# Kernel tuning notes

Hardware: AMD Instinct MI355X
Metric: run time of the kernel (lower is better)

## Reference

```python
import jax, jax.numpy as jnp
import numpy as np

NEG_SLOPE = 0.2  # leaky_relu negative slope (alpha)

def _glorot(key, shape):
    fan_in, fan_out = shape[0], shape[-1]
    lim = jnp.sqrt(6.0 / (fan_in + fan_out))
    return jax.random.uniform(key, shape, jnp.float32, -lim, lim)

def setup_inputs() -> dict:
    key = jax.random.key(0)
    ks = jax.random.split(key, 10)
    N, E, F_IN, HID, HEADS, NCLASS = 50000, 800000, 512, 32, 8, 32
    x = jax.random.normal(ks[0], (N, F_IN), jnp.float32)
    edge_index = jax.random.randint(ks[1], (2, E), 0, N, jnp.int64)
    # layer 1: heads=8, out per head = 32, concat -> 256
    W1 = _glorot(ks[2], (F_IN, HEADS * HID))
    att_src1 = _glorot(ks[3], (HEADS, HID))
    att_dst1 = _glorot(ks[4], (HEADS, HID))
    b1 = jnp.zeros((HEADS * HID,), jnp.float32)
    # layer 2: heads=1, out = nclass
    W2 = _glorot(ks[5], (HEADS * HID, NCLASS))
    att_src2 = _glorot(ks[6], (1, NCLASS))
    att_dst2 = _glorot(ks[7], (1, NCLASS))
    b2 = jnp.zeros((NCLASS,), jnp.float32)
    return {"x": x, "edge_index": edge_index, "W1": W1, "att_src1": att_src1,
            "att_dst1": att_dst1, "b1": b1, "W2": W2, "att_src2": att_src2,
            "att_dst2": att_dst2, "b2": b2}

def gat_conv(x, src, dst, W, a_src, a_dst, bias, num_nodes):
    """PyG GATConv (eval mode, self loops already appended to src/dst)."""
    H, C = a_src.shape
    h = (x @ W).reshape(num_nodes, H, C)                 # [N,H,C]
    score_src = jnp.einsum('nhc,hc->nh', h, a_src)       # [N,H]
    score_dst = jnp.einsum('nhc,hc->nh', h, a_dst)       # [N,H]
    e = jax.nn.leaky_relu(score_src[src] + score_dst[dst], NEG_SLOPE)  # [E,H]
    m = jax.ops.segment_max(e, dst, num_segments=num_nodes)           # [N,H]
    w = jnp.exp(e - m[dst])
    denom = jax.ops.segment_sum(w, dst, num_segments=num_nodes)       # [N,H]
    alpha = w / (denom[dst] + 1e-16)                                  # [E,H]
    out = jax.ops.segment_sum(alpha[:, :, None] * h[src], dst,
                              num_segments=num_nodes)                 # [N,H,C]
    return out.reshape(num_nodes, H * C) + bias

def reference(x, edge_index, W1, att_src1, att_dst1, b1, W2, att_src2, att_dst2, b2):
    N = x.shape[0]
    loops = jnp.arange(N, dtype=edge_index.dtype)
    src = jnp.concatenate([edge_index[0], loops])  # PyG add_self_loops=True
    dst = jnp.concatenate([edge_index[1], loops])
    h = jax.nn.elu(gat_conv(x, src, dst, W1, att_src1, att_dst1, b1, N))
    out = gat_conv(h, src, dst, W2, att_src2, att_dst2, b2, N)
    return out + 1e-06
```

## Files before the change

### kernel.cpp

```cpp
#include <hip/hip_runtime.h>
#include <math.h>

#define N_NODES 50000
#define N_EDGES 800000
#define E2 (N_EDGES + N_NODES)
#define F_IN 512
#define HEADS 8
#define HID 32
#define HC 256
#define NCLASS 32
#define NEG_SLOPE 0.2f
#define ELLW 64

typedef unsigned int uint;
typedef unsigned short ushort;
typedef __attribute__((ext_vector_type(8))) short bf16x8;
typedef __attribute__((ext_vector_type(4))) float f32x4;

#define GLOBAL_LOAD_LDS16(g, l) \
    __builtin_amdgcn_global_load_lds((const __attribute__((address_space(1))) void*)(g), \
                                     (__attribute__((address_space(3))) void*)(l), 16, 0, 0)

__device__ inline uint bf16_rne_bits(float f) {
    uint u = __float_as_uint(f);
    return (u + 0x7fffu + ((u >> 16) & 1u)) >> 16;
}
__device__ inline float bf2f(ushort u) { return __uint_as_float(((uint)u) << 16); }

#define W1_BLOCKS 512
#define W2_BLOCKS 32
#define FILL_BLOCKS ((E2 / 4 + 255) / 256)

__global__ void __launch_bounds__(256) prep_kernel(const float* __restrict__ W1,
        ushort* __restrict__ w1hi, ushort* __restrict__ w1lo,
        const float* __restrict__ W2, ushort* __restrict__ w2hi, ushort* __restrict__ w2lo,
        const int* __restrict__ ei, int* __restrict__ cursor, int* __restrict__ ell) {
    int b = blockIdx.x;
    if (b < W1_BLOCKS) {
        int t = b * 256 + threadIdx.x;
        int n = t >> 9, k = t & 511;
        float f = W1[k * 256 + n];
        uint h = bf16_rne_bits(f);
        float r = f - __uint_as_float(h << 16);
        w1hi[t] = (ushort)h;
        w1lo[t] = (ushort)bf16_rne_bits(r);
    } else if (b < W1_BLOCKS + W2_BLOCKS) {
        int t = (b - W1_BLOCKS) * 256 + threadIdx.x;
        int n = t >> 8, k = t & 255;
        float f = W2[k * 32 + n];
        uint h = bf16_rne_bits(f);
        float r = f - __uint_as_float(h << 16);
        w2hi[t] = (ushort)h;
        w2lo[t] = (ushort)bf16_rne_bits(r);
    } else {
        int e0 = ((b - W1_BLOCKS - W2_BLOCKS) * 256 + threadIdx.x) * 4;
        if (e0 < E2) {
            int src[4], dst[4];
            if (e0 < N_EDGES) {
                int4 s4 = *(const int4*)(ei + e0);
                int4 d4 = *(const int4*)(ei + N_EDGES + e0);
                src[0] = s4.x; src[1] = s4.y; src[2] = s4.z; src[3] = s4.w;
                dst[0] = d4.x; dst[1] = d4.y; dst[2] = d4.z; dst[3] = d4.w;
            } else {
                #pragma unroll
                for (int j = 0; j < 4; ++j) { src[j] = e0 + j - N_EDGES; dst[j] = src[j]; }
            }
            #pragma unroll
            for (int j = 0; j < 4; ++j) {
                int d = dst[j];
                int p = atomicAdd(&cursor[d], 1);
                ell[d * ELLW + p] = src[j];
            }
        }
    }
}

__global__ void __launch_bounds__(256, 4) gemm1_mfma_kernel(const uint* __restrict__ xp,
        const ushort* __restrict__ bhi, const ushort* __restrict__ blo,
        const float* __restrict__ as1, const float* __restrict__ ad1,
        ushort* __restrict__ C, float* __restrict__ ssrc, float* __restrict__ sdst, int M) {
    __shared__ uint   As[64 * 32];
    __shared__ ushort Bh[128 * 32];
    __shared__ ushort Bl[128 * 32];
    const int tid = threadIdx.x, lane = tid & 63, wave = tid >> 6;

    const int NW = ((N_NODES + 63) / 64) * 2;
    const int orig = blockIdx.y * gridDim.x + blockIdx.x;
    const int xcd = orig & 7, idx = orig >> 3;
    const int q = NW >> 3, r = NW & 7;
    const int nid = (xcd < r ? xcd * (q + 1) : r * (q + 1) + (xcd - r) * q) + idx;
    const int bm = (nid >> 1) * 64, bn = (nid & 1) * 128;

    const uint* agp[2]; const uint* alp[2];
    #pragma unroll
    for (int s = 0; s < 2; ++s) {
        int t = wave * 2 + s;
        int p = t * 64 + lane;
        int row = p >> 3, cs = p & 7;
        int c = cs ^ (row & 7);
        int grow = bm + row; if (grow > M - 1) grow = M - 1;
        agp[s] = xp + ((size_t)grow * 512 + c * 4);
        alp[s] = &As[t * 256];
    }
    const ushort* bhgp[2]; const ushort* blgp[2]; const ushort* bhlp[2]; const ushort* bllp[2];
    #pragma unroll
    for (int s = 0; s < 2; ++s) {
        int t = wave * 2 + s;
        int p = t * 64 + lane;
        int row = p >> 2, qs = p & 3;
        int qq = qs ^ ((row >> 1) & 3);
        size_t go = (size_t)(bn + row) * 512 + qq * 8;
        bhgp[s] = bhi + go; blgp[s] = blo + go;
        bhlp[s] = &Bh[t * 512]; bllp[s] = &Bl[t * 512];
    }

    f32x4 acc[2][4] = {};
    const int wm = (wave >> 1) * 32, wn = (wave & 1) * 64;
    const int fm = lane & 15, quad = lane >> 4;

    for (int kk = 0; kk < 16; ++kk) {
        #pragma unroll
        for (int s = 0; s < 2; ++s) GLOBAL_LOAD_LDS16(agp[s], alp[s]);
        #pragma unroll
        for (int s = 0; s < 2; ++s) {
            GLOBAL_LOAD_LDS16(bhgp[s], bhlp[s]);
            GLOBAL_LOAD_LDS16(blgp[s], bllp[s]);
        }
        #pragma unroll
        for (int s = 0; s < 2; ++s) { agp[s] += 32; bhgp[s] += 32; blgp[s] += 32; }
        __syncthreads();

        bf16x8 ah[2], al[2], bh[4], bl[4];
        #pragma unroll
        for (int i = 0; i < 2; ++i) {
            int row = wm + i * 16 + fm;
            int sw = row & 7;
            uint4 c0 = *(const uint4*)&As[row * 32 + (((2 * quad)     ^ sw) * 4)];
            uint4 c1 = *(const uint4*)&As[row * 32 + (((2 * quad + 1) ^ sw) * 4)];
            union { uint u[4]; bf16x8 v; } H, L;
            H.u[0] = __builtin_amdgcn_perm(c0.y, c0.x, 0x07060302u);
            H.u[1] = __builtin_amdgcn_perm(c0.w, c0.z, 0x07060302u);
            H.u[2] = __builtin_amdgcn_perm(c1.y, c1.x, 0x07060302u);
            H.u[3] = __builtin_amdgcn_perm(c1.w, c1.z, 0x07060302u);
            uint r0 = __float_as_uint(__uint_as_float(c0.x) - __uint_as_float(c0.x & 0xffff0000u));
            uint r1 = __float_as_uint(__uint_as_float(c0.y) - __uint_as_float(c0.y & 0xffff0000u));
            uint r2 = __float_as_uint(__uint_as_float(c0.z) - __uint_as_float(c0.z & 0xffff0000u));
            uint r3 = __float_as_uint(__uint_as_float(c0.w) - __uint_as_float(c0.w & 0xffff0000u));
            uint r4 = __float_as_uint(__uint_as_float(c1.x) - __uint_as_float(c1.x & 0xffff0000u));
            uint r5 = __float_as_uint(__uint_as_float(c1.y) - __uint_as_float(c1.y & 0xffff0000u));
            uint r6 = __float_as_uint(__uint_as_float(c1.z) - __uint_as_float(c1.z & 0xffff0000u));
            uint r7 = __float_as_uint(__uint_as_float(c1.w) - __uint_as_float(c1.w & 0xffff0000u));
            L.u[0] = __builtin_amdgcn_perm(r1, r0, 0x07060302u);
            L.u[1] = __builtin_amdgcn_perm(r3, r2, 0x07060302u);
            L.u[2] = __builtin_amdgcn_perm(r5, r4, 0x07060302u);
            L.u[3] = __builtin_amdgcn_perm(r7, r6, 0x07060302u);
            ah[i] = H.v; al[i] = L.v;
        }
        #pragma unroll
        for (int j = 0; j < 4; ++j) {
            int row = wn + j * 16 + fm;
            int qs = quad ^ ((row >> 1) & 3);
            bh[j] = *(const bf16x8*)&Bh[row * 32 + qs * 8];
            bl[j] = *(const bf16x8*)&Bl[row * 32 + qs * 8];
        }
        #pragma unroll
        for (int i = 0; i < 2; ++i)
            #pragma unroll
            for (int j = 0; j < 4; ++j) {
                acc[i][j] = __builtin_amdgcn_mfma_f32_16x16x32_bf16(ah[i], bh[j], acc[i][j], 0, 0, 0);
                acc[i][j] = __builtin_amdgcn_mfma_f32_16x16x32_bf16(ah[i], bl[j], acc[i][j], 0, 0, 0);
                acc[i][j] = __builtin_amdgcn_mfma_f32_16x16x32_bf16(al[i], bh[j], acc[i][j], 0, 0, 0);
            }
        __syncthreads();
    }

    #pragma unroll
    for (int i = 0; i < 2; ++i) {
        int rb = bm + wm + i * 16 + quad * 4;
        #pragma unroll
        for (int j = 0; j < 4; ++j) {
            int col = bn + wn + j * 16 + fm;
            #pragma unroll
            for (int r2_ = 0; r2_ < 4; ++r2_) {
                int row = rb + r2_;
                if (row < M) C[(size_t)row * 256 + col] = (ushort)bf16_rne_bits(acc[i][j][r2_]);
            }
        }
    }

    const int head0 = (bn + wn) >> 5;
    const float asA0 = as1[head0 * 32 + fm],      asA1 = as1[head0 * 32 + 16 + fm];
    const float asB0 = as1[head0 * 32 + 32 + fm], asB1 = as1[head0 * 32 + 48 + fm];
    const float adA0 = ad1[head0 * 32 + fm],      adA1 = ad1[head0 * 32 + 16 + fm];
    const float adB0 = ad1[head0 * 32 + 32 + fm], adB1 = ad1[head0 * 32 + 48 + fm];
    #pragma unroll
    for (int i = 0; i < 2; ++i) {
        #pragma unroll
        for (int r2_ = 0; r2_ < 4; ++r2_) {
            int row = bm + wm + i * 16 + quad * 4 + r2_;
            float s1A = acc[i][0][r2_] * asA0 + acc[i][1][r2_] * asA1;
            float s1B = acc[i][2][r2_] * asB0 + acc[i][3][r2_] * asB1;
            float s2A = acc[i][0][r2_] * adA0 + acc[i][1][r2_] * adA1;
            float s2B = acc[i][2][r2_] * adB0 + acc[i][3][r2_] * adB1;
            #pragma unroll
            for (int off = 1; off < 16; off <<= 1) {
                s1A += __shfl_xor(s1A, off);
                s1B += __shfl_xor(s1B, off);
                s2A += __shfl_xor(s2A, off);
                s2B += __shfl_xor(s2B, off);
            }
            if (fm == 0 && row < M) {
                ssrc[(size_t)row * 8 + head0]     = s1A;
                ssrc[(size_t)row * 8 + head0 + 1] = s1B;
                sdst[(size_t)row * 8 + head0]     = s2A;
                sdst[(size_t)row * 8 + head0 + 1] = s2B;
            }
        }
    }
}

__global__ void __launch_bounds__(256) gemm2_mfma_kernel(const ushort* __restrict__ A,
        const ushort* __restrict__ bh_g, const ushort* __restrict__ bl_g,
        const float* __restrict__ as2, const float* __restrict__ ad2,
        ushort* __restrict__ C, float* __restrict__ ssrc, float* __restrict__ sdst, int M) {
    const int tid = threadIdx.x, lane = tid & 63, wave = tid >> 6;
    const int bm = blockIdx.x * 128;
    const int fm = lane & 15, quad = lane >> 4;
    const int wrow = wave * 32;

    int gr[2];
    #pragma unroll
    for (int i = 0; i < 2; ++i) {
        gr[i] = bm + wrow + i * 16 + fm;
        if (gr[i] > M - 1) gr[i] = M - 1;
    }

    f32x4 acc[2][2] = {};
    for (int kk = 0; kk < 8; ++kk) {
        bf16x8 a[2], bh[2], bl[2];
        #pragma unroll
        for (int i = 0; i < 2; ++i)
            a[i] = *(const bf16x8*)(A + (size_t)gr[i] * 256 + kk * 32 + quad * 8);
        #pragma unroll
        for (int j = 0; j < 2; ++j) {
            size_t off = (size_t)(j * 16 + fm) * 256 + kk * 32 + quad * 8;
            bh[j] = *(const bf16x8*)(bh_g + off);
            bl[j] = *(const bf16x8*)(bl_g + off);
        }
        #pragma unroll
        for (int i = 0; i < 2; ++i)
            #pragma unroll
            for (int j = 0; j < 2; ++j) {
                acc[i][j] = __builtin_amdgcn_mfma_f32_16x16x32_bf16(a[i], bh[j], acc[i][j], 0, 0, 0);
                acc[i][j] = __builtin_amdgcn_mfma_f32_16x16x32_bf16(a[i], bl[j], acc[i][j], 0, 0, 0);
            }
    }

    float a0 = as2[fm], a1 = as2[16 + fm];
    float d0 = ad2[fm], d1 = ad2[16 + fm];
    #pragma unroll
    for (int i = 0; i < 2; ++i) {
        #pragma unroll
        for (int r2_ = 0; r2_ < 4; ++r2_) {
            int rg = bm + wrow + i * 16 + quad * 4 + r2_;
            float v0 = acc[i][0][r2_], v1 = acc[i][1][r2_];
            float s1 = v0 * a0 + v1 * a1;
            float s2 = v0 * d0 + v1 * d1;
            #pragma unroll
            for (int off = 1; off < 16; off <<= 1) {
                s1 += __shfl_xor(s1, off);
                s2 += __shfl_xor(s2, off);
            }
            if (rg < M) {
                C[(size_t)rg * 32 + fm]      = (ushort)bf16_rne_bits(v0);
                C[(size_t)rg * 32 + 16 + fm] = (ushort)bf16_rne_bits(v1);
                if (fm == 0) { ssrc[rg] = s1; sdst[rg] = s2; }
            }
        }
    }
}

__global__ void __launch_bounds__(256) agg1_wave_kernel(const ushort* __restrict__ h,
        const float* __restrict__ ssrc, const float* __restrict__ sdst,
        const int* __restrict__ cnt, const int* __restrict__ ell,
        const float* __restrict__ bias, ushort* __restrict__ out) {
    const int wid = (blockIdx.x * blockDim.x + threadIdx.x) >> 6;
    if (wid >= N_NODES) return;
    const int lane = threadIdx.x & 63;
    const int hg = lane >> 3;
    const int hl = lane & 7;
    const int n = wid;
    const int beg = n * ELLW;
    const int end = beg + cnt[n];
    const float sdst_n = sdst[(size_t)n * HEADS + hg];

    float4 acc = make_float4(0.f, 0.f, 0.f, 0.f);
    float sw = 0.f;
    const ushort* hc = h + lane * 4;
    const int base = hg << 3;
    for (int e = beg; e < end; e += 16) {
        int ee0 = e + hl, ee1 = e + 8 + hl;
        int ei0 = ee0 < end ? ee0 : end - 1;
        int ei1 = ee1 < end ? ee1 : end - 1;
        int s0 = ell[ei0];
        int s1 = ell[ei1];
        float c0 = ssrc[(size_t)s0 * HEADS + hg] + sdst_n;
        float c1 = ssrc[(size_t)s1 * HEADS + hg] + sdst_n;
        c0 = c0 > 0.f ? c0 : NEG_SLOPE * c0;
        c1 = c1 > 0.f ? c1 : NEG_SLOPE * c1;
        float w0 = (ee0 < end) ? __expf(c0) : 0.f;
        float w1 = (ee1 < end) ? __expf(c1) : 0.f;
        float wj[16]; int sj[16];
        #pragma unroll
        for (int j = 0; j < 8; ++j) {
            wj[j]     = __shfl(w0, base + j);
            sj[j]     = __shfl(s0, base + j);
            wj[8 + j] = __shfl(w1, base + j);
            sj[8 + j] = __shfl(s1, base + j);
        }
        ushort4 v[16];
        #pragma unroll
        for (int j = 0; j < 16; ++j) v[j] = *(const ushort4*)(hc + (size_t)sj[j] * HC);
        #pragma unroll
        for (int j = 0; j < 16; ++j) {
            acc.x += wj[j] * bf2f(v[j].x);
            acc.y += wj[j] * bf2f(v[j].y);
            acc.z += wj[j] * bf2f(v[j].z);
            acc.w += wj[j] * bf2f(v[j].w);
            sw += wj[j];
        }
    }
    float inv = 1.f / (sw + 1e-16f);
    float4 bv = *(const float4*)(bias + lane * 4);
    float4 o;
    o.x = acc.x * inv + bv.x; o.y = acc.y * inv + bv.y;
    o.z = acc.z * inv + bv.z; o.w = acc.w * inv + bv.w;
    o.x = o.x > 0.f ? o.x : expm1f(o.x);
    o.y = o.y > 0.f ? o.y : expm1f(o.y);
    o.z = o.z > 0.f ? o.z : expm1f(o.z);
    o.w = o.w > 0.f ? o.w : expm1f(o.w);
    ushort4 ob;
    ob.x = (ushort)bf16_rne_bits(o.x);
    ob.y = (ushort)bf16_rne_bits(o.y);
    ob.z = (ushort)bf16_rne_bits(o.z);
    ob.w = (ushort)bf16_rne_bits(o.w);
    *(ushort4*)(out + (size_t)n * HC + lane * 4) = ob;
}

__global__ void __launch_bounds__(256) agg2_kernel(const ushort* __restrict__ h2,
        const float* __restrict__ ssrc, const float* __restrict__ sdst,
        const int* __restrict__ cnt, const int* __restrict__ ell,
        const float* __restrict__ bias, float* __restrict__ out) {
    const int n = blockIdx.x * 4 + (threadIdx.x >> 6);
    if (n >= N_NODES) return;
    const int beg = n * ELLW;
    const int end = beg + cnt[n];
    const int t = threadIdx.x & 63;
    const float sdst_n = sdst[n];

    const int slot = t >> 4, cp = t & 15;
    float a0 = 0.f, a1 = 0.f, sw = 0.f;
    for (int e = beg + slot; e < end; e += 4) {
        int src = ell[e];
        float sc = ssrc[src] + sdst_n;
        sc = sc > 0.f ? sc : NEG_SLOPE * sc;
        float w = __expf(sc);
        uint v = *(const uint*)(h2 + (size_t)src * NCLASS + cp * 2);
        a0 += w * __uint_as_float(v << 16);
        a1 += w * __uint_as_float(v & 0xffff0000u);
        sw += w;
    }
    a0 += __shfl_down(a0, 32); a1 += __shfl_down(a1, 32); sw += __shfl_down(sw, 32);
    a0 += __shfl_down(a0, 16); a1 += __shfl_down(a1, 16); sw += __shfl_down(sw, 16);
    if (t < 16) {
        float inv = 1.f / (sw + 1e-16f);
        float2 o;
        o.x = a0 * inv + bias[cp * 2]     + 1e-6f;
        o.y = a1 * inv + bias[cp * 2 + 1] + 1e-6f;
        *(float2*)(out + (size_t)n * NCLASS + cp * 2) = o;
    }
}

extern "C" void kernel_launch(void* const* d_in, const int* in_sizes, int n_in,
                              void* d_out, int out_size, void* d_ws, size_t ws_size,
                              hipStream_t stream) {
    const float* x        = (const float*)d_in[0];
    const int*   ei       = (const int*)  d_in[1];
    const float* W1       = (const float*)d_in[2];
    const float* att_src1 = (const float*)d_in[3];
    const float* att_dst1 = (const float*)d_in[4];
    const float* b1       = (const float*)d_in[5];
    const float* W2       = (const float*)d_in[6];
    const float* att_src2 = (const float*)d_in[7];
    const float* att_dst2 = (const float*)d_in[8];
    const float* b2       = (const float*)d_in[9];
    float* out = (float*)d_out;

    ushort* w1t_hi = (ushort*)d_ws;
    ushort* w1t_lo = w1t_hi + 256 * 512;
    ushort* w2t_hi = w1t_lo + 256 * 512;
    ushort* w2t_lo = w2t_hi + 32 * 256;
    ushort* h1b    = w2t_lo + 32 * 256;
    ushort* h2b    = h1b + (size_t)N_NODES * HC;
    ushort* out1b  = h2b + (size_t)N_NODES * NCLASS;
    float* ssrc1 = (float*)(out1b + (size_t)N_NODES * HC);
    float* sdst1 = ssrc1 + (size_t)N_NODES * HEADS;
    float* ssrc2 = sdst1 + (size_t)N_NODES * HEADS;
    float* sdst2 = ssrc2 + N_NODES;
    int* cursor  = (int*)(sdst2 + N_NODES);
    int* ell     = cursor + N_NODES;

    hipMemsetAsync(cursor, 0, N_NODES * sizeof(int), stream);
    prep_kernel<<<W1_BLOCKS + W2_BLOCKS + FILL_BLOCKS, 256, 0, stream>>>(
            W1, w1t_hi, w1t_lo, W2, w2t_hi, w2t_lo, ei, cursor, ell);

    {
        dim3 grid((N_NODES + 63) / 64, 2);
        gemm1_mfma_kernel<<<grid, 256, 0, stream>>>((const uint*)x, w1t_hi, w1t_lo,
                att_src1, att_dst1, h1b, ssrc1, sdst1, N_NODES);
    }
    agg1_wave_kernel<<<(N_NODES + 3) / 4, 256, 0, stream>>>(h1b, ssrc1, sdst1, cursor, ell, b1, out1b);

    gemm2_mfma_kernel<<<(N_NODES + 127) / 128, 256, 0, stream>>>(out1b, w2t_hi, w2t_lo,
            att_src2, att_dst2, h2b, ssrc2, sdst2, N_NODES);
    agg2_kernel<<<(N_NODES + 3) / 4, 256, 0, stream>>>(h2b, ssrc2, sdst2, cursor, ell, b2, out);
}
```

Measured before the change: 374.9 us.

## Enlarge GEMM1 tile, shrink GEMM2 tile, split agg1 tail loop

GEMM1 moves from 64x256-column tiles to 128-row tiles, so each wave computes a 64x64 sub-block and each loaded B tile is reused across twice as many rows, and the occupancy hint of 4 is dropped. GEMM2 goes the other way: each wave handles 16 rows instead of 32 and twice as many blocks are launched, giving more parallelism for the small 32-column output. The layer-1 aggregation loop is split into a mask-free main body over full 16-edge chunks plus a guarded tail that loads only the edges still needed, avoiding clamped duplicate gathers. The costs are higher register pressure and lower occupancy in GEMM1, and less per-wave reuse of W2 in GEMM2.

```diff
diff --git a/kernel.cpp b/kernel.cpp
--- a/kernel.cpp
+++ b/kernel.cpp
@@ -75,26 +75,26 @@
     }
 }
 
-__global__ void __launch_bounds__(256, 4) gemm1_mfma_kernel(const uint* __restrict__ xp,
+__global__ void __launch_bounds__(256) gemm1_mfma_kernel(const uint* __restrict__ xp,
         const ushort* __restrict__ bhi, const ushort* __restrict__ blo,
         const float* __restrict__ as1, const float* __restrict__ ad1,
         ushort* __restrict__ C, float* __restrict__ ssrc, float* __restrict__ sdst, int M) {
-    __shared__ uint   As[64 * 32];
+    __shared__ uint   As[128 * 32];
     __shared__ ushort Bh[128 * 32];
     __shared__ ushort Bl[128 * 32];
     const int tid = threadIdx.x, lane = tid & 63, wave = tid >> 6;
 
-    const int NW = ((N_NODES + 63) / 64) * 2;
+    const int NW = ((N_NODES + 127) / 128) * 2;
     const int orig = blockIdx.y * gridDim.x + blockIdx.x;
     const int xcd = orig & 7, idx = orig >> 3;
     const int q = NW >> 3, r = NW & 7;
     const int nid = (xcd < r ? xcd * (q + 1) : r * (q + 1) + (xcd - r) * q) + idx;
-    const int bm = (nid >> 1) * 64, bn = (nid & 1) * 128;
-
-    const uint* agp[2]; const uint* alp[2];
+    const int bm = (nid >> 1) * 128, bn = (nid & 1) * 128;
+
+    const uint* agp[4]; const uint* alp[4];
     #pragma unroll
-    for (int s = 0; s < 2; ++s) {
-        int t = wave * 2 + s;
+    for (int s = 0; s < 4; ++s) {
+        int t = wave * 4 + s;
         int p = t * 64 + lane;
         int row = p >> 3, cs = p & 7;
         int c = cs ^ (row & 7);
@@ -114,25 +114,27 @@
         bhlp[s] = &Bh[t * 512]; bllp[s] = &Bl[t * 512];
     }
 
-    f32x4 acc[2][4] = {};
-    const int wm = (wave >> 1) * 32, wn = (wave & 1) * 64;
+    f32x4 acc[4][4] = {};
+    const int wm = (wave >> 1) * 64, wn = (wave & 1) * 64;
     const int fm = lane & 15, quad = lane >> 4;
 
     for (int kk = 0; kk < 16; ++kk) {
         #pragma unroll
-        for (int s = 0; s < 2; ++s) GLOBAL_LOAD_LDS16(agp[s], alp[s]);
+        for (int s = 0; s < 4; ++s) GLOBAL_LOAD_LDS16(agp[s], alp[s]);
         #pragma unroll
         for (int s = 0; s < 2; ++s) {
             GLOBAL_LOAD_LDS16(bhgp[s], bhlp[s]);
             GLOBAL_LOAD_LDS16(blgp[s], bllp[s]);
         }
         #pragma unroll
-        for (int s = 0; s < 2; ++s) { agp[s] += 32; bhgp[s] += 32; blgp[s] += 32; }
+        for (int s = 0; s < 4; ++s) agp[s] += 32;
+        #pragma unroll
+        for (int s = 0; s < 2; ++s) { bhgp[s] += 32; blgp[s] += 32; }
         __syncthreads();
 
-        bf16x8 ah[2], al[2], bh[4], bl[4];
-        #pragma unroll
-        for (int i = 0; i < 2; ++i) {
+        bf16x8 ah[4], al[4], bh[4], bl[4];
+        #pragma unroll
+        for (int i = 0; i < 4; ++i) {
             int row = wm + i * 16 + fm;
             int sw = row & 7;
             uint4 c0 = *(const uint4*)&As[row * 32 + (((2 * quad)     ^ sw) * 4)];
@@ -164,7 +166,7 @@
             bl[j] = *(const bf16x8*)&Bl[row * 32 + qs * 8];
         }
         #pragma unroll
-        for (int i = 0; i < 2; ++i)
+        for (int i = 0; i < 4; ++i)
             #pragma unroll
             for (int j = 0; j < 4; ++j) {
                 acc[i][j] = __builtin_amdgcn_mfma_f32_16x16x32_bf16(ah[i], bh[j], acc[i][j], 0, 0, 0);
@@ -175,7 +177,7 @@
     }
 
     #pragma unroll
-    for (int i = 0; i < 2; ++i) {
+    for (int i = 0; i < 4; ++i) {
         int rb = bm + wm + i * 16 + quad * 4;
         #pragma unroll
         for (int j = 0; j < 4; ++j) {
@@ -194,7 +196,7 @@
     const float adA0 = ad1[head0 * 32 + fm],      adA1 = ad1[head0 * 32 + 16 + fm];
     const float adB0 = ad1[head0 * 32 + 32 + fm], adB1 = ad1[head0 * 32 + 48 + fm];
     #pragma unroll
-    for (int i = 0; i < 2; ++i) {
+    for (int i = 0; i < 4; ++i) {
         #pragma unroll
         for (int r2_ = 0; r2_ < 4; ++r2_) {
             int row = bm + wm + i * 16 + quad * 4 + r2_;
@@ -224,23 +226,16 @@
         const float* __restrict__ as2, const float* __restrict__ ad2,
         ushort* __restrict__ C, float* __restrict__ ssrc, float* __restrict__ sdst, int M) {
     const int tid = threadIdx.x, lane = tid & 63, wave = tid >> 6;
-    const int bm = blockIdx.x * 128;
+    const int bm = blockIdx.x * 64;
     const int fm = lane & 15, quad = lane >> 4;
-    const int wrow = wave * 32;
-
-    int gr[2];
-    #pragma unroll
-    for (int i = 0; i < 2; ++i) {
-        gr[i] = bm + wrow + i * 16 + fm;
-        if (gr[i] > M - 1) gr[i] = M - 1;
-    }
-
-    f32x4 acc[2][2] = {};
+    const int wrow = wave * 16;
+
+    int gr = bm + wrow + fm; if (gr > M - 1) gr = M - 1;
+
+    f32x4 acc[2] = {};
     for (int kk = 0; kk < 8; ++kk) {
-        bf16x8 a[2], bh[2], bl[2];
-        #pragma unroll
-        for (int i = 0; i < 2; ++i)
-            a[i] = *(const bf16x8*)(A + (size_t)gr[i] * 256 + kk * 32 + quad * 8);
+        bf16x8 a, bh[2], bl[2];
+        a = *(const bf16x8*)(A + (size_t)gr * 256 + kk * 32 + quad * 8);
         #pragma unroll
         for (int j = 0; j < 2; ++j) {
             size_t off = (size_t)(j * 16 + fm) * 256 + kk * 32 + quad * 8;
@@ -248,34 +243,29 @@
             bl[j] = *(const bf16x8*)(bl_g + off);
         }
         #pragma unroll
-        for (int i = 0; i < 2; ++i)
-            #pragma unroll
-            for (int j = 0; j < 2; ++j) {
-                acc[i][j] = __builtin_amdgcn_mfma_f32_16x16x32_bf16(a[i], bh[j], acc[i][j], 0, 0, 0);
-                acc[i][j] = __builtin_amdgcn_mfma_f32_16x16x32_bf16(a[i], bl[j], acc[i][j], 0, 0, 0);
-            }
+        for (int j = 0; j < 2; ++j) {
+            acc[j] = __builtin_amdgcn_mfma_f32_16x16x32_bf16(a, bh[j], acc[j], 0, 0, 0);
+            acc[j] = __builtin_amdgcn_mfma_f32_16x16x32_bf16(a, bl[j], acc[j], 0, 0, 0);
+        }
     }
 
     float a0 = as2[fm], a1 = as2[16 + fm];
     float d0 = ad2[fm], d1 = ad2[16 + fm];
     #pragma unroll
-    for (int i = 0; i < 2; ++i) {
-        #pragma unroll
-        for (int r2_ = 0; r2_ < 4; ++r2_) {
-            int rg = bm + wrow + i * 16 + quad * 4 + r2_;
-            float v0 = acc[i][0][r2_], v1 = acc[i][1][r2_];
-            float s1 = v0 * a0 + v1 * a1;
-            float s2 = v0 * d0 + v1 * d1;
-            #pragma unroll
-            for (int off = 1; off < 16; off <<= 1) {
-                s1 += __shfl_xor(s1, off);
-                s2 += __shfl_xor(s2, off);
-            }
-            if (rg < M) {
-                C[(size_t)rg * 32 + fm]      = (ushort)bf16_rne_bits(v0);
-                C[(size_t)rg * 32 + 16 + fm] = (ushort)bf16_rne_bits(v1);
-                if (fm == 0) { ssrc[rg] = s1; sdst[rg] = s2; }
-            }
+    for (int r2_ = 0; r2_ < 4; ++r2_) {
+        int rg = bm + wrow + quad * 4 + r2_;
+        float v0 = acc[0][r2_], v1 = acc[1][r2_];
+        float s1 = v0 * a0 + v1 * a1;
+        float s2 = v0 * d0 + v1 * d1;
+        #pragma unroll
+        for (int off = 1; off < 16; off <<= 1) {
+            s1 += __shfl_xor(s1, off);
+            s2 += __shfl_xor(s2, off);
+        }
+        if (rg < M) {
+            C[(size_t)rg * 32 + fm]      = (ushort)bf16_rne_bits(v0);
+            C[(size_t)rg * 32 + 16 + fm] = (ushort)bf16_rne_bits(v1);
+            if (fm == 0) { ssrc[rg] = s1; sdst[rg] = s2; }
         }
     }
 }
@@ -298,7 +288,39 @@
     float sw = 0.f;
     const ushort* hc = h + lane * 4;
     const int base = hg << 3;
-    for (int e = beg; e < end; e += 16) {
+
+    int e = beg;
+    for (; e + 16 <= end; e += 16) {
+        int s0 = ell[e + hl];
+        int s1 = ell[e + 8 + hl];
+        float c0 = ssrc[(size_t)s0 * HEADS + hg] + sdst_n;
+        float c1 = ssrc[(size_t)s1 * HEADS + hg] + sdst_n;
+        c0 = c0 > 0.f ? c0 : NEG_SLOPE * c0;
+        c1 = c1 > 0.f ? c1 : NEG_SLOPE * c1;
+        float w0 = __expf(c0);
+        float w1 = __expf(c1);
+        float wj[16]; int sj[16];
+        #pragma unroll
+        for (int j = 0; j < 8; ++j) {
+            wj[j]     = __shfl(w0, base + j);
+            sj[j]     = __shfl(s0, base + j);
+            wj[8 + j] = __shfl(w1, base + j);
+            sj[8 + j] = __shfl(s1, base + j);
+        }
+        ushort4 v[16];
+        #pragma unroll
+        for (int j = 0; j < 16; ++j) v[j] = *(const ushort4*)(hc + (size_t)sj[j] * HC);
+        #pragma unroll
+        for (int j = 0; j < 16; ++j) {
+            acc.x += wj[j] * bf2f(v[j].x);
+            acc.y += wj[j] * bf2f(v[j].y);
+            acc.z += wj[j] * bf2f(v[j].z);
+            acc.w += wj[j] * bf2f(v[j].w);
+            sw += wj[j];
+        }
+    }
+    if (e < end) {
+        const int rem = end - e;
         int ee0 = e + hl, ee1 = e + 8 + hl;
         int ei0 = ee0 < end ? ee0 : end - 1;
         int ei1 = ee1 < end ? ee1 : end - 1;
@@ -318,18 +340,19 @@
             wj[8 + j] = __shfl(w1, base + j);
             sj[8 + j] = __shfl(s1, base + j);
         }
-        ushort4 v[16];
-        #pragma unroll
-        for (int j = 0; j < 16; ++j) v[j] = *(const ushort4*)(hc + (size_t)sj[j] * HC);
         #pragma unroll
         for (int j = 0; j < 16; ++j) {
-            acc.x += wj[j] * bf2f(v[j].x);
-            acc.y += wj[j] * bf2f(v[j].y);
-            acc.z += wj[j] * bf2f(v[j].z);
-            acc.w += wj[j] * bf2f(v[j].w);
-            sw += wj[j];
-        }
-    }
+            if (j < rem) {
+                ushort4 v = *(const ushort4*)(hc + (size_t)sj[j] * HC);
+                acc.x += wj[j] * bf2f(v.x);
+                acc.y += wj[j] * bf2f(v.y);
+                acc.z += wj[j] * bf2f(v.z);
+                acc.w += wj[j] * bf2f(v.w);
+                sw += wj[j];
+            }
+        }
+    }
+
     float inv = 1.f / (sw + 1e-16f);
     float4 bv = *(const float4*)(bias + lane * 4);
     float4 o;
@@ -415,13 +438,13 @@
             W1, w1t_hi, w1t_lo, W2, w2t_hi, w2t_lo, ei, cursor, ell);
 
     {
-        dim3 grid((N_NODES + 63) / 64, 2);
+        dim3 grid((N_NODES + 127) / 128, 2);
         gemm1_mfma_kernel<<<grid, 256, 0, stream>>>((const uint*)x, w1t_hi, w1t_lo,
                 att_src1, att_dst1, h1b, ssrc1, sdst1, N_NODES);
     }
     agg1_wave_kernel<<<(N_NODES + 3) / 4, 256, 0, stream>>>(h1b, ssrc1, sdst1, cursor, ell, b1, out1b);
 
-    gemm2_mfma_kernel<<<(N_NODES + 127) / 128, 256, 0, stream>>>(out1b, w2t_hi, w2t_lo,
+    gemm2_mfma_kernel<<<(N_NODES + 63) / 64, 256, 0, stream>>>(out1b, w2t_hi, w2t_lo,
             att_src2, att_dst2, h2b, ssrc2, sdst2, N_NODES);
     agg2_kernel<<<(N_NODES + 3) / 4, 256, 0, stream>>>(h2b, ssrc2, sdst2, cursor, ell, b2, out);
 }
```

New measurement: 382.8 us. 2.1% more time.
